# Kernel optimization log

Measured on AMD Instinct MI355X. Metric: run time of the kernel, lower is better.

The kernel has to match this reference:

```python
import jax, jax.numpy as jnp
import numpy as np

B, L, D, M = 4, 8192, 512, 256
EPS = 1e-6


def _feature_map(x, proj, is_query):
    # FAVOR+ positive softmax-kernel features.
    # x: (B, L, D), proj: (M, D) with orthogonal rows scaled by sqrt(D).
    d = x.shape[-1]
    xs = x * (d ** -0.25)                      # scale by d^{-1/4}
    dash = jnp.einsum('bld,md->blm', xs, proj)  # (B, L, M)
    diag = 0.5 * jnp.sum(xs * xs, axis=-1, keepdims=True)  # (B, L, 1)
    if is_query:
        stab = jnp.max(dash, axis=-1, keepdims=True)        # per-position max
    else:
        stab = jnp.max(dash, axis=(-2, -1), keepdims=True)  # per-batch max
    return jnp.exp(dash - diag - stab) / jnp.sqrt(jnp.asarray(M, x.dtype)) + EPS


def setup_inputs() -> dict:
    key = jax.random.key(0)
    kq, kk, kv, kp = jax.random.split(key, 4)
    Q = jax.random.normal(kq, (B, L, D), dtype=jnp.float32)
    K = jax.random.normal(kk, (B, L, D), dtype=jnp.float32)
    V = jax.random.normal(kv, (B, L, D), dtype=jnp.float32)
    # Orthogonal random projection: QR of a Gaussian, rows scaled by sqrt(D).
    G = jax.random.normal(kp, (D, M), dtype=jnp.float32)
    q, _ = jnp.linalg.qr(G)                     # (D, M), orthonormal columns
    proj = q.T * jnp.sqrt(jnp.asarray(D, jnp.float32))  # (M, D)
    return {"Q": Q, "K": K, "V": V, "proj": proj}


def reference(Q, K, V, proj):
    Qf = _feature_map(Q, proj, is_query=True)   # (B, L, M)
    Kf = _feature_map(K, proj, is_query=False)  # (B, L, M)
    # Linear attention: aggregate keys/values once, O(L*M*D).
    KV = jnp.einsum('blm,bld->bmd', Kf, V)      # (B, M, D)
    Ksum = jnp.sum(Kf, axis=1)                  # (B, M)
    Z = 1.0 / (jnp.einsum('blm,bm->bl', Qf, Ksum) + EPS)  # (B, L)
    out = jnp.einsum('blm,bmd->bld', Qf, KV) * Z[..., None]
    return out
```

## Files before the change

kernel.cpp:

```cpp
#include <hip/hip_runtime.h>
#include <math.h>

typedef unsigned short u16;
typedef unsigned int u32;
typedef __attribute__((ext_vector_type(8))) short bf16x8;
typedef __attribute__((ext_vector_type(4))) float f32x4;

#define SCALE_ 0.21022410381342864f
#define EPS_ 1e-6f
#define RSQM_ 0.0625f
#define L_ 8192
#define PL_OFF_ 131072
#define KVL_OFF_ 524288

__device__ __forceinline__ float bf2f(u16 h) {
    return __uint_as_float(((u32)h) << 16);
}
__device__ __forceinline__ u32 cvtpk(float x0, float x1) {
    u32 w;
    asm("v_cvt_pk_bf16_f32 %0, %1, %2" : "=v"(w) : "v"(x0), "v"(x1));
    return w;
}
__device__ __forceinline__ void split_pk(float x0, float x1, u32& hw, u32& lw) {
    hw = cvtpk(x0, x1);
    float h0 = __uint_as_float(hw << 16);
    float h1 = __uint_as_float(hw & 0xffff0000u);
    lw = cvtpk(x0 - h0, x1 - h1);
}
__device__ __forceinline__ u32 okey(float x) {
    u32 b = __float_as_uint(x);
    return (b & 0x80000000u) ? ~b : (b | 0x80000000u);
}
__device__ __forceinline__ float odec(u32 k) {
    return (k & 0x80000000u) ? __uint_as_float(k & 0x7fffffffu) : __uint_as_float(~k);
}

#define GLDS16(gsrc, ldst) \
    __builtin_amdgcn_global_load_lds((__attribute__((address_space(1))) void*)(gsrc), \
                                     (__attribute__((address_space(3))) void*)(ldst), 16, 0, 0)

__global__ __launch_bounds__(256) void split_p(const float* __restrict__ P,
        u16* __restrict__ Ph, u16* __restrict__ Pl, u32* __restrict__ bmax) {
    if (blockIdx.x == 0 && threadIdx.x < 4) bmax[threadIdx.x] = 0u;
    int i = (blockIdx.x * 256 + threadIdx.x) * 2;
    u32 hw, lw;
    split_pk(P[i] * SCALE_, P[i + 1] * SCALE_, hw, lw);
    *reinterpret_cast<u32*>(&Ph[i]) = hw;
    *reinterpret_cast<u32*>(&Pl[i]) = lw;
}

__global__ __launch_bounds__(256) void dash_all(
        const float* __restrict__ Qg, const float* __restrict__ Kg,
        const u16* __restrict__ Bh_g,
        u16* __restrict__ QF, u16* __restrict__ KfT, float* __restrict__ ksump,
        u32* __restrict__ bmax) {
    __shared__ __align__(16) u16 Ah[2][64 * 32], Al[2][64 * 32];
    __shared__ __align__(16) u16 Bh[2][256 * 32], Bl[2][256 * 32];
    const int qpath = !(blockIdx.x & 1);
    const int tile = blockIdx.x >> 1;
    const float* __restrict__ X = qpath ? Qg : Kg;
    const int t = threadIdx.x, lane = t & 63;
    const int wid = t >> 6;
    const int row0 = tile * 64;
    const int l15 = lane & 15, l4 = lane >> 4;
    const int sr = t >> 2;
    const int awz = sr * 32 + (((t & 3) ^ ((sr >> 1) & 3)) * 8);
    const int koff = (l4 ^ ((l15 >> 1) & 3)) * 8;
    float ss = 0.f;

    const float* xp = &X[(size_t)(row0 + sr) * 512 + (t & 3) * 8];
    const u16* bsrch[4];
#pragma unroll
    for (int it = 0; it < 4; ++it) {
        const int m = it * 64 + wid * 16 + (lane >> 2);
        const int swz = ((lane & 3) ^ ((m >> 1) & 3)) * 8;
        bsrch[it] = Bh_g + (size_t)m * 512 + swz;
    }

    f32x4 acc[4][4];
#pragma unroll
    for (int i = 0; i < 4; ++i)
#pragma unroll
        for (int j = 0; j < 4; ++j) acc[i][j] = (f32x4){0.f, 0.f, 0.f, 0.f};

    float4 v0 = *reinterpret_cast<const float4*>(xp);
    float4 v1 = *reinterpret_cast<const float4*>(xp + 4);
    float4 v2 = *reinterpret_cast<const float4*>(xp + 32);
    float4 v3 = *reinterpret_cast<const float4*>(xp + 36);

    for (int kt = 0; kt < 8; ++kt) {
        __syncthreads();
        {
#pragma unroll
            for (int it = 0; it < 4; ++it) {
                GLDS16(bsrch[it],                 &Bh[0][it * 2048 + wid * 512]);
                GLDS16(bsrch[it] + PL_OFF_,       &Bl[0][it * 2048 + wid * 512]);
                GLDS16(bsrch[it] + 32,            &Bh[1][it * 2048 + wid * 512]);
                GLDS16(bsrch[it] + 32 + PL_OFF_,  &Bl[1][it * 2048 + wid * 512]);
                bsrch[it] += 64;
            }
            float xs[8] = {v0.x, v0.y, v0.z, v0.w, v1.x, v1.y, v1.z, v1.w};
            float ys[8] = {v2.x, v2.y, v2.z, v2.w, v3.x, v3.y, v3.z, v3.w};
#pragma unroll
            for (int i = 0; i < 8; ++i) {
                ss = fmaf(xs[i], xs[i], ss);
                ss = fmaf(ys[i], ys[i], ss);
            }
            u32 hw[4], lw[4];
#pragma unroll
            for (int i = 0; i < 4; ++i) split_pk(xs[2 * i], xs[2 * i + 1], hw[i], lw[i]);
            *reinterpret_cast<uint4*>(&Ah[0][awz]) = make_uint4(hw[0], hw[1], hw[2], hw[3]);
            *reinterpret_cast<uint4*>(&Al[0][awz]) = make_uint4(lw[0], lw[1], lw[2], lw[3]);
#pragma unroll
            for (int i = 0; i < 4; ++i) split_pk(ys[2 * i], ys[2 * i + 1], hw[i], lw[i]);
            *reinterpret_cast<uint4*>(&Ah[1][awz]) = make_uint4(hw[0], hw[1], hw[2], hw[3]);
            *reinterpret_cast<uint4*>(&Al[1][awz]) = make_uint4(lw[0], lw[1], lw[2], lw[3]);
            xp = (kt < 7) ? xp + 64 : xp;
            v0 = *reinterpret_cast<const float4*>(xp);
            v1 = *reinterpret_cast<const float4*>(xp + 4);
            v2 = *reinterpret_cast<const float4*>(xp + 32);
            v3 = *reinterpret_cast<const float4*>(xp + 36);
        }
        __syncthreads();
#pragma unroll
        for (int h = 0; h < 2; ++h) {
            bf16x8 a_h[4], a_l[4];
#pragma unroll
            for (int mf = 0; mf < 4; ++mf) {
                int r = (mf * 16 + l15) * 32 + koff;
                a_h[mf] = *reinterpret_cast<const bf16x8*>(&Ah[h][r]);
                a_l[mf] = *reinterpret_cast<const bf16x8*>(&Al[h][r]);
            }
#pragma unroll
            for (int nf = 0; nf < 4; ++nf) {
                const int r = (wid * 64 + nf * 16 + l15) * 32 + koff;
                bf16x8 b_h = *reinterpret_cast<const bf16x8*>(&Bh[h][r]);
                bf16x8 b_l = *reinterpret_cast<const bf16x8*>(&Bl[h][r]);
#pragma unroll
                for (int mf = 0; mf < 4; ++mf) {
                    acc[mf][nf] = __builtin_amdgcn_mfma_f32_16x16x32_bf16(a_h[mf], b_h, acc[mf][nf], 0, 0, 0);
                    acc[mf][nf] = __builtin_amdgcn_mfma_f32_16x16x32_bf16(a_h[mf], b_l, acc[mf][nf], 0, 0, 0);
                    acc[mf][nf] = __builtin_amdgcn_mfma_f32_16x16x32_bf16(a_l[mf], b_h, acc[mf][nf], 0, 0, 0);
                }
            }
        }
    }
    __syncthreads();
    float* rmaxp = reinterpret_cast<float*>(&Ah[0][0]);
    float* diagp = reinterpret_cast<float*>(&Al[0][0]);

    ss += __shfl_xor(ss, 1);
    ss += __shfl_xor(ss, 2);
    if ((t & 3) == 0) diagp[sr] = 0.5f * SCALE_ * SCALE_ * ss;

    if (qpath) {
        float rm[4][4];
#pragma unroll
        for (int mf = 0; mf < 4; ++mf)
#pragma unroll
            for (int r = 0; r < 4; ++r) {
                float v = fmaxf(fmaxf(acc[mf][0][r], acc[mf][1][r]),
                                fmaxf(acc[mf][2][r], acc[mf][3][r]));
#pragma unroll
                for (int off = 1; off < 16; off <<= 1) v = fmaxf(v, __shfl_xor(v, off));
                rm[mf][r] = v;
            }
        if (l15 == 0) {
#pragma unroll
            for (int mf = 0; mf < 4; ++mf)
#pragma unroll
                for (int r = 0; r < 4; ++r)
                    rmaxp[(mf * 16 + l4 * 4 + r) * 4 + wid] = rm[mf][r];
        }
        __syncthreads();
#pragma unroll
        for (int mf = 0; mf < 4; ++mf)
#pragma unroll
            for (int r = 0; r < 4; ++r) {
                const int rl = mf * 16 + l4 * 4 + r;
                float m4 = fmaxf(fmaxf(rmaxp[rl * 4 + 0], rmaxp[rl * 4 + 1]),
                                 fmaxf(rmaxp[rl * 4 + 2], rmaxp[rl * 4 + 3]));
                const float c = diagp[rl] + m4;
                float f0 = expf(acc[mf][0][r] - c) * RSQM_ + EPS_;
                float f1 = expf(acc[mf][1][r] - c) * RSQM_ + EPS_;
                float f2 = expf(acc[mf][2][r] - c) * RSQM_ + EPS_;
                float f3 = expf(acc[mf][3][r] - c) * RSQM_ + EPS_;
                u32 w01 = cvtpk(f0, f1), w23 = cvtpk(f2, f3);
                size_t o = (size_t)(row0 + rl) * 256 + wid * 64 + l15;
                QF[o]      = (u16)w01;
                QF[o + 16] = (u16)(w01 >> 16);
                QF[o + 32] = (u16)w23;
                QF[o + 48] = (u16)(w23 >> 16);
            }
    } else {
        __syncthreads();
        const int b = row0 >> 13;
        const int ll = row0 & 8191;
        float bm = -1e30f;
        float s[4] = {0.f, 0.f, 0.f, 0.f};
#pragma unroll
        for (int nf = 0; nf < 4; ++nf) {
            const size_t mb = ((size_t)(b * 256 + wid * 64 + nf * 16 + l15)) * 8192 + ll + l4 * 4;
#pragma unroll
            for (int mf = 0; mf < 4; ++mf) {
                float e0 = acc[mf][nf][0], e1 = acc[mf][nf][1];
                float e2 = acc[mf][nf][2], e3 = acc[mf][nf][3];
                bm = fmaxf(fmaxf(bm, fmaxf(e0, e1)), fmaxf(e2, e3));
                float x0 = expf(e0 - diagp[mf * 16 + l4 * 4 + 0]);
                float x1 = expf(e1 - diagp[mf * 16 + l4 * 4 + 1]);
                float x2 = expf(e2 - diagp[mf * 16 + l4 * 4 + 2]);
                float x3 = expf(e3 - diagp[mf * 16 + l4 * 4 + 3]);
                s[nf] += (x0 + x1) + (x2 + x3);
                uint2 w = make_uint2(cvtpk(x0, x1), cvtpk(x2, x3));
                *reinterpret_cast<uint2*>(&KfT[mb + mf * 16]) = w;
            }
        }
#pragma unroll
        for (int nf = 0; nf < 4; ++nf) {
            s[nf] += __shfl_xor(s[nf], 16);
            s[nf] += __shfl_xor(s[nf], 32);
        }
        if (l4 == 0) {
#pragma unroll
            for (int nf = 0; nf < 4; ++nf)
                ksump[tile * 256 + wid * 64 + nf * 16 + l15] = s[nf];
        }
#pragma unroll
        for (int off = 1; off < 64; off <<= 1) bm = fmaxf(bm, __shfl_xor(bm, off));
        if (lane == 0) diagp[64 + wid] = bm;
        __syncthreads();
        if (t == 0) {
            float m = fmaxf(fmaxf(diagp[64], diagp[65]), fmaxf(diagp[66], diagp[67]));
            atomicMax(&bmax[b], okey(m));
        }
    }
}

__global__ __launch_bounds__(256) void split_vt(const float* __restrict__ V,
        u16* __restrict__ Vt, float* __restrict__ vsump) {
    const int dt = blockIdx.x & 7, lt = blockIdx.x >> 3;
    const int lg = lt * 64, b = lg >> 13, d0 = dt * 64;
    __shared__ u16 T[64][72];
    const int t = threadIdx.x;
    const int lrow = t >> 2, c0 = (t & 3) * 16;
#pragma unroll
    for (int ii = 0; ii < 4; ++ii) {
        float4 v = *reinterpret_cast<const float4*>(&V[(size_t)(lg + lrow) * 512 + d0 + c0 + ii * 4]);
        *reinterpret_cast<u32*>(&T[lrow][c0 + ii * 4 + 0]) = cvtpk(v.x, v.y);
        *reinterpret_cast<u32*>(&T[lrow][c0 + ii * 4 + 2]) = cvtpk(v.z, v.w);
    }
    __syncthreads();
    const int dloc = t >> 2, lc = (t & 3) * 16;
    u32 w[8];
    float s = 0.f;
#pragma unroll
    for (int j = 0; j < 8; ++j) {
        u16 a = T[lc + 2 * j][dloc], c = T[lc + 2 * j + 1][dloc];
        w[j] = (u32)a | ((u32)c << 16);
        s += bf2f(a) + bf2f(c);
    }
    size_t ob = ((size_t)(b * 512 + d0 + dloc)) * 8192 + (lg & 8191) + lc;
    reinterpret_cast<uint4*>(&Vt[ob])[0] = make_uint4(w[0], w[1], w[2], w[3]);
    reinterpret_cast<uint4*>(&Vt[ob])[1] = make_uint4(w[4], w[5], w[6], w[7]);
    s += __shfl_xor(s, 1);
    s += __shfl_xor(s, 2);
    if ((t & 3) == 0) vsump[lt * 512 + d0 + dloc] = s;
}

__global__ __launch_bounds__(256) void ksum_red(const float* __restrict__ ksump,
        const u32* __restrict__ bmax, float* __restrict__ KsumT) {
    const int wid = threadIdx.x >> 6, lane = threadIdx.x & 63;
    const int o = blockIdx.x * 4 + wid;
    const int b = o >> 8, m = o & 255;
    float s = ksump[(size_t)(b * 128 + lane) * 256 + m]
            + ksump[(size_t)(b * 128 + 64 + lane) * 256 + m];
#pragma unroll
    for (int off = 1; off < 64; off <<= 1) s += __shfl_xor(s, off);
    if (lane == 0) {
        const float g = expf(-odec(bmax[b]));
        KsumT[o] = g * s + (float)L_ * EPS_;
    }
}

__global__ __launch_bounds__(256) void vsum_red(const float* __restrict__ vsump,
        float* __restrict__ Vsum) {
    const int wid = threadIdx.x >> 6, lane = threadIdx.x & 63;
    const int o = blockIdx.x * 4 + wid;
    const int b = o >> 9, d = o & 511;
    float s = vsump[(size_t)(b * 128 + lane) * 512 + d]
            + vsump[(size_t)(b * 128 + 64 + lane) * 512 + d];
#pragma unroll
    for (int off = 1; off < 64; off <<= 1) s += __shfl_xor(s, off);
    if (lane == 0) Vsum[o] = s;
}

__global__ __launch_bounds__(256) void kv_mfma(
        const u16* __restrict__ KfT, const u16* __restrict__ Vt,
        float* __restrict__ kvp) {
    int o = (blockIdx.x & 7) * 64 + (blockIdx.x >> 3);
    const int dt = o & 3, mt = (o >> 2) & 1, ch = (o >> 3) & 15, b = o >> 7;
    const u16* Ag = KfT + ((size_t)(b * 256 + mt * 128)) * 8192 + ch * 512;
    const u16* Bg = Vt + ((size_t)(b * 512 + dt * 128)) * 8192 + ch * 512;
    __shared__ __align__(16) u16 A_[2][128 * 32], B_[2][128 * 32];
    const int t = threadIdx.x, lane = t & 63;
    const int wid = t >> 6, wr = wid >> 1, wc = wid & 1;
    const int l15 = lane & 15, l4 = lane >> 4;
    const int koff = (l4 ^ ((l15 >> 1) & 3)) * 8;
    const u16* asrc[2];
    const u16* bsrc[2];
#pragma unroll
    for (int it = 0; it < 2; ++it) {
        const int row = it * 64 + wid * 16 + (lane >> 2);
        const int swz = ((lane & 3) ^ ((row >> 1) & 3)) * 8;
        asrc[it] = Ag + (size_t)row * 8192 + swz;
        bsrc[it] = Bg + (size_t)row * 8192 + swz;
    }
    f32x4 acc[4][4];
#pragma unroll
    for (int i = 0; i < 4; ++i)
#pragma unroll
        for (int j = 0; j < 4; ++j) acc[i][j] = (f32x4){0.f, 0.f, 0.f, 0.f};

    for (int kt = 0; kt < 8; ++kt) {
        __syncthreads();
#pragma unroll
        for (int it = 0; it < 2; ++it) {
            GLDS16(asrc[it],      &A_[0][it * 2048 + wid * 512]);
            GLDS16(asrc[it] + 32, &A_[1][it * 2048 + wid * 512]);
            GLDS16(bsrc[it],      &B_[0][it * 2048 + wid * 512]);
            GLDS16(bsrc[it] + 32, &B_[1][it * 2048 + wid * 512]);
            asrc[it] += 64; bsrc[it] += 64;
        }
        __syncthreads();
#pragma unroll
        for (int h = 0; h < 2; ++h) {
            bf16x8 a[4];
#pragma unroll
            for (int mf = 0; mf < 4; ++mf)
                a[mf] = *reinterpret_cast<const bf16x8*>(&A_[h][(wr * 64 + mf * 16 + l15) * 32 + koff]);
#pragma unroll
            for (int nf = 0; nf < 4; ++nf) {
                bf16x8 bb = *reinterpret_cast<const bf16x8*>(&B_[h][(wc * 64 + nf * 16 + l15) * 32 + koff]);
#pragma unroll
                for (int mf = 0; mf < 4; ++mf)
                    acc[mf][nf] = __builtin_amdgcn_mfma_f32_16x16x32_bf16(a[mf], bb, acc[mf][nf], 0, 0, 0);
            }
        }
    }
#pragma unroll
    for (int mf = 0; mf < 4; ++mf)
#pragma unroll
        for (int r = 0; r < 4; ++r) {
            size_t oo = ((size_t)(ch * 4 + b) * 256 + mt * 128 + wr * 64 + mf * 16 + l4 * 4 + r) * 512
                        + dt * 128 + wc * 64;
#pragma unroll
            for (int nf = 0; nf < 4; ++nf)
                kvp[oo + nf * 16 + l15] = acc[mf][nf][r];
        }
}

__global__ __launch_bounds__(256) void kv_fix(const float* __restrict__ kvp,
        const u32* __restrict__ bmax, const float* __restrict__ Vsum,
        u16* __restrict__ KVth, u16* __restrict__ KVtl) {
    const int dt = blockIdx.x & 7, mt = (blockIdx.x >> 3) & 3, b = blockIdx.x >> 5;
    const int m0 = mt * 64, d0 = dt * 64;
    __shared__ u16 Th[64][72], Tl[64][72];
    const int t = threadIdx.x, mloc = t >> 2, c0 = (t & 3) * 16;
    float s[16];
#pragma unroll
    for (int j = 0; j < 16; ++j) s[j] = 0.f;
    for (int c = 0; c < 16; ++c) {
        size_t base = ((size_t)(c * 4 + b) * 256 + m0 + mloc) * 512 + d0 + c0;
#pragma unroll
        for (int ii = 0; ii < 4; ++ii) {
            float4 v = *reinterpret_cast<const float4*>(&kvp[base + ii * 4]);
            s[ii * 4 + 0] += v.x; s[ii * 4 + 1] += v.y;
            s[ii * 4 + 2] += v.z; s[ii * 4 + 3] += v.w;
        }
    }
    const float g = expf(-odec(bmax[b]));
#pragma unroll
    for (int j = 0; j < 16; j += 2) {
        float v0 = g * s[j]     + EPS_ * Vsum[b * 512 + d0 + c0 + j];
        float v1 = g * s[j + 1] + EPS_ * Vsum[b * 512 + d0 + c0 + j + 1];
        u32 hw, lw; split_pk(v0, v1, hw, lw);
        *reinterpret_cast<u32*>(&Th[mloc][c0 + j]) = hw;
        *reinterpret_cast<u32*>(&Tl[mloc][c0 + j]) = lw;
    }
    __syncthreads();
    const int dloc = t >> 2, mc = (t & 3) * 16;
    size_t ob = ((size_t)(b * 512 + d0 + dloc)) * 256 + m0 + mc;
    u32 wh[8], wl[8];
#pragma unroll
    for (int j = 0; j < 8; ++j) {
        wh[j] = (u32)Th[mc + 2 * j][dloc] | ((u32)Th[mc + 2 * j + 1][dloc] << 16);
        wl[j] = (u32)Tl[mc + 2 * j][dloc] | ((u32)Tl[mc + 2 * j + 1][dloc] << 16);
    }
    reinterpret_cast<uint4*>(&KVth[ob])[0] = make_uint4(wh[0], wh[1], wh[2], wh[3]);
    reinterpret_cast<uint4*>(&KVth[ob])[1] = make_uint4(wh[4], wh[5], wh[6], wh[7]);
    reinterpret_cast<uint4*>(&KVtl[ob])[0] = make_uint4(wl[0], wl[1], wl[2], wl[3]);
    reinterpret_cast<uint4*>(&KVtl[ob])[1] = make_uint4(wl[4], wl[5], wl[6], wl[7]);
}

__global__ __launch_bounds__(256) void z_kernel(const u16* __restrict__ QF,
        const float* __restrict__ KsumT, float* __restrict__ Z) {
    const int wid = threadIdx.x >> 6, lane = threadIdx.x & 63;
    const int row = blockIdx.x * 4 + wid;
    const int b = row >> 13;
    uint2 u = *reinterpret_cast<const uint2*>(&QF[(size_t)row * 256 + lane * 4]);
    float4 ks = *reinterpret_cast<const float4*>(&KsumT[b * 256 + lane * 4]);
    float s = bf2f((u16)(u.x & 0xffff)) * ks.x + bf2f((u16)(u.x >> 16)) * ks.y +
              bf2f((u16)(u.y & 0xffff)) * ks.z + bf2f((u16)(u.y >> 16)) * ks.w;
#pragma unroll
    for (int off = 1; off < 64; off <<= 1) s += __shfl_xor(s, off);
    if (lane == 0) Z[row] = 1.f / (s + EPS_);
}

__global__ __launch_bounds__(256) void out_mfma(
        const u16* __restrict__ QF, const u16* __restrict__ KVth,
        const float* __restrict__ Z, float* __restrict__ out) {
    int o = (blockIdx.x & 7) * 128 + (blockIdx.x >> 3);
    const int dt = o & 3, rt = o >> 2;
    const int row0 = rt * 128, b = row0 >> 13;
    const u16* Ag = QF + (size_t)row0 * 256;
    const u16* Bh_g = KVth + ((size_t)(b * 512 + dt * 128)) * 256;
    __shared__ __align__(16) u16 A_[2][128 * 32], Bh_[2][128 * 32], Bl_[2][128 * 32];
    const int t = threadIdx.x, lane = t & 63;
    const int wid = t >> 6, wr = wid >> 1, wc = wid & 1;
    const int l15 = lane & 15, l4 = lane >> 4;
    const int koff = (l4 ^ ((l15 >> 1) & 3)) * 8;
    const u16* asrc[2];
    const u16* bhsrc[2];
#pragma unroll
    for (int it = 0; it < 2; ++it) {
        const int row = it * 64 + wid * 16 + (lane >> 2);
        const int swz = ((lane & 3) ^ ((row >> 1) & 3)) * 8;
        asrc[it]  = Ag + (size_t)row * 256 + swz;
        bhsrc[it] = Bh_g + (size_t)row * 256 + swz;
    }
    f32x4 acc[4][4];
#pragma unroll
    for (int i = 0; i < 4; ++i)
#pragma unroll
        for (int j = 0; j < 4; ++j) acc[i][j] = (f32x4){0.f, 0.f, 0.f, 0.f};

    for (int kt = 0; kt < 4; ++kt) {
        __syncthreads();
#pragma unroll
        for (int it = 0; it < 2; ++it) {
            GLDS16(asrc[it],                  &A_[0][it * 2048 + wid * 512]);
            GLDS16(asrc[it] + 32,             &A_[1][it * 2048 + wid * 512]);
            GLDS16(bhsrc[it],                 &Bh_[0][it * 2048 + wid * 512]);
            GLDS16(bhsrc[it] + 32,            &Bh_[1][it * 2048 + wid * 512]);
            GLDS16(bhsrc[it] + KVL_OFF_,      &Bl_[0][it * 2048 + wid * 512]);
            GLDS16(bhsrc[it] + 32 + KVL_OFF_, &Bl_[1][it * 2048 + wid * 512]);
            asrc[it] += 64; bhsrc[it] += 64;
        }
        __syncthreads();
#pragma unroll
        for (int h = 0; h < 2; ++h) {
            bf16x8 a[4];
#pragma unroll
            for (int mf = 0; mf < 4; ++mf)
                a[mf] = *reinterpret_cast<const bf16x8*>(&A_[h][(wr * 64 + mf * 16 + l15) * 32 + koff]);
#pragma unroll
            for (int nf = 0; nf < 4; ++nf) {
                const int r = (wc * 64 + nf * 16 + l15) * 32 + koff;
                bf16x8 bh = *reinterpret_cast<const bf16x8*>(&Bh_[h][r]);
                bf16x8 bl = *reinterpret_cast<const bf16x8*>(&Bl_[h][r]);
#pragma unroll
                for (int mf = 0; mf < 4; ++mf) {
                    acc[mf][nf] = __builtin_amdgcn_mfma_f32_16x16x32_bf16(a[mf], bh, acc[mf][nf], 0, 0, 0);
                    acc[mf][nf] = __builtin_amdgcn_mfma_f32_16x16x32_bf16(a[mf], bl, acc[mf][nf], 0, 0, 0);
                }
            }
        }
    }
#pragma unroll
    for (int mf = 0; mf < 4; ++mf)
#pragma unroll
        for (int r = 0; r < 4; ++r) {
            const int row = row0 + wr * 64 + mf * 16 + l4 * 4 + r;
            const float z = Z[row];
#pragma unroll
            for (int nf = 0; nf < 4; ++nf)
                out[(size_t)row * 512 + dt * 128 + wc * 64 + nf * 16 + l15] = acc[mf][nf][r] * z;
        }
}

extern "C" void kernel_launch(void* const* d_in, const int* in_sizes, int n_in,
                              void* d_out, int out_size, void* d_ws, size_t ws_size,
                              hipStream_t stream) {
    const float* Q = (const float*)d_in[0];
    const float* K = (const float*)d_in[1];
    const float* V = (const float*)d_in[2];
    const float* P = (const float*)d_in[3];
    float* out = (float*)d_out;
    char* ws = (char*)d_ws;

    u16*   QF    = (u16*)(ws + 0);
    u16*   KfT   = (u16*)(ws + 16777216);
    u16*   Vt    = (u16*)(ws + 33554432);
    float* kvp   = (float*)(ws + 67108864);
    u16*   KVth  = (u16*)(ws + 100663296);
    u16*   KVtl  = (u16*)(ws + 101711872);
    u16*   PH    = (u16*)(ws + 102760448);
    u16*   PL    = (u16*)(ws + 103022592);
    float* ksump = (float*)(ws + 103284736);
    float* vsump = (float*)(ws + 103809024);
    float* KsumT = (float*)(ws + 104857600);
    float* Vsum  = (float*)(ws + 104861696);
    float* Zbuf  = (float*)(ws + 104869888);
    u32*   bmax  = (u32*)(ws + 105000960);

    split_p<<<256, 256, 0, stream>>>(P, PH, PL, bmax);
    dash_all<<<1024, 256, 0, stream>>>(Q, K, PH, QF, KfT, ksump, bmax);
    split_vt<<<4096, 256, 0, stream>>>(V, Vt, vsump);
    ksum_red<<<256, 256, 0, stream>>>(ksump, bmax, KsumT);
    vsum_red<<<512, 256, 0, stream>>>(vsump, Vsum);
    kv_mfma<<<512, 256, 0, stream>>>(KfT, Vt, kvp);
    kv_fix<<<128, 256, 0, stream>>>(kvp, bmax, Vsum, KVth, KVtl);
    z_kernel<<<8192, 256, 0, stream>>>(QF, KsumT, Zbuf);
    out_mfma<<<1024, 256, 0, stream>>>(QF, KVth, Zbuf, out);
}
```

Baseline: 160.8 us.

## Fuse V transpose/bf16 conversion and V-sum into kv_mfma B-tile loading

Removes the separate split_vt kernel that transposed V into a bf16 Vt buffer. kv_mfma now reads fp32 V directly, converts pairs to bf16 and writes them swizzled into the LDS B tile, while also accumulating per-column V sums. A small vsum_red reduces the per-chunk partials. This eliminates a full write and re-read of the transposed V (about 32 MB of traffic) and one launch. In exchange, the B-tile load becomes synchronous register loads with scattered 4-byte LDS stores instead of async global-to-LDS copies, and V is read twice, once by each mt tile.

```diff
diff --git a/kernel.cpp b/kernel.cpp
--- a/kernel.cpp
+++ b/kernel.cpp
@@ -236,37 +236,6 @@
     }
 }
 
-__global__ __launch_bounds__(256) void split_vt(const float* __restrict__ V,
-        u16* __restrict__ Vt, float* __restrict__ vsump) {
-    const int dt = blockIdx.x & 7, lt = blockIdx.x >> 3;
-    const int lg = lt * 64, b = lg >> 13, d0 = dt * 64;
-    __shared__ u16 T[64][72];
-    const int t = threadIdx.x;
-    const int lrow = t >> 2, c0 = (t & 3) * 16;
-#pragma unroll
-    for (int ii = 0; ii < 4; ++ii) {
-        float4 v = *reinterpret_cast<const float4*>(&V[(size_t)(lg + lrow) * 512 + d0 + c0 + ii * 4]);
-        *reinterpret_cast<u32*>(&T[lrow][c0 + ii * 4 + 0]) = cvtpk(v.x, v.y);
-        *reinterpret_cast<u32*>(&T[lrow][c0 + ii * 4 + 2]) = cvtpk(v.z, v.w);
-    }
-    __syncthreads();
-    const int dloc = t >> 2, lc = (t & 3) * 16;
-    u32 w[8];
-    float s = 0.f;
-#pragma unroll
-    for (int j = 0; j < 8; ++j) {
-        u16 a = T[lc + 2 * j][dloc], c = T[lc + 2 * j + 1][dloc];
-        w[j] = (u32)a | ((u32)c << 16);
-        s += bf2f(a) + bf2f(c);
-    }
-    size_t ob = ((size_t)(b * 512 + d0 + dloc)) * 8192 + (lg & 8191) + lc;
-    reinterpret_cast<uint4*>(&Vt[ob])[0] = make_uint4(w[0], w[1], w[2], w[3]);
-    reinterpret_cast<uint4*>(&Vt[ob])[1] = make_uint4(w[4], w[5], w[6], w[7]);
-    s += __shfl_xor(s, 1);
-    s += __shfl_xor(s, 2);
-    if ((t & 3) == 0) vsump[lt * 512 + d0 + dloc] = s;
-}
-
 __global__ __launch_bounds__(256) void ksum_red(const float* __restrict__ ksump,
         const u32* __restrict__ bmax, float* __restrict__ KsumT) {
     const int wid = threadIdx.x >> 6, lane = threadIdx.x & 63;
@@ -282,39 +251,29 @@
     }
 }
 
-__global__ __launch_bounds__(256) void vsum_red(const float* __restrict__ vsump,
-        float* __restrict__ Vsum) {
-    const int wid = threadIdx.x >> 6, lane = threadIdx.x & 63;
-    const int o = blockIdx.x * 4 + wid;
-    const int b = o >> 9, d = o & 511;
-    float s = vsump[(size_t)(b * 128 + lane) * 512 + d]
-            + vsump[(size_t)(b * 128 + 64 + lane) * 512 + d];
-#pragma unroll
-    for (int off = 1; off < 64; off <<= 1) s += __shfl_xor(s, off);
-    if (lane == 0) Vsum[o] = s;
-}
-
 __global__ __launch_bounds__(256) void kv_mfma(
-        const u16* __restrict__ KfT, const u16* __restrict__ Vt,
-        float* __restrict__ kvp) {
+        const u16* __restrict__ KfT, const float* __restrict__ V,
+        float* __restrict__ kvp, float* __restrict__ vsump) {
     int o = (blockIdx.x & 7) * 64 + (blockIdx.x >> 3);
     const int dt = o & 3, mt = (o >> 2) & 1, ch = (o >> 3) & 15, b = o >> 7;
     const u16* Ag = KfT + ((size_t)(b * 256 + mt * 128)) * 8192 + ch * 512;
-    const u16* Bg = Vt + ((size_t)(b * 512 + dt * 128)) * 8192 + ch * 512;
+    const float* Vg = V + ((size_t)(b * 8192 + ch * 512)) * 512 + dt * 128;
     __shared__ __align__(16) u16 A_[2][128 * 32], B_[2][128 * 32];
     const int t = threadIdx.x, lane = t & 63;
     const int wid = t >> 6, wr = wid >> 1, wc = wid & 1;
     const int l15 = lane & 15, l4 = lane >> 4;
     const int koff = (l4 ^ ((l15 >> 1) & 3)) * 8;
     const u16* asrc[2];
-    const u16* bsrc[2];
 #pragma unroll
     for (int it = 0; it < 2; ++it) {
         const int row = it * 64 + wid * 16 + (lane >> 2);
         const int swz = ((lane & 3) ^ ((row >> 1) & 3)) * 8;
         asrc[it] = Ag + (size_t)row * 8192 + swz;
-        bsrc[it] = Bg + (size_t)row * 8192 + swz;
-    }
+    }
+    const int dq = t >> 3;
+    const int lpb = (t & 7) * 2;
+    float vs[4] = {0.f, 0.f, 0.f, 0.f};
+
     f32x4 acc[4][4];
 #pragma unroll
     for (int i = 0; i < 4; ++i)
@@ -327,10 +286,29 @@
         for (int it = 0; it < 2; ++it) {
             GLDS16(asrc[it],      &A_[0][it * 2048 + wid * 512]);
             GLDS16(asrc[it] + 32, &A_[1][it * 2048 + wid * 512]);
-            GLDS16(bsrc[it],      &B_[0][it * 2048 + wid * 512]);
-            GLDS16(bsrc[it] + 32, &B_[1][it * 2048 + wid * 512]);
-            asrc[it] += 64; bsrc[it] += 64;
-        }
+            asrc[it] += 64;
+        }
+#pragma unroll
+        for (int h = 0; h < 2; ++h)
+#pragma unroll
+            for (int j = 0; j < 2; ++j) {
+                const int lp = lpb + j;
+                const int l = kt * 64 + h * 32 + lp * 2;
+                const float* vp = Vg + (size_t)l * 512 + dq * 4;
+                float4 va = *reinterpret_cast<const float4*>(vp);
+                float4 vb = *reinterpret_cast<const float4*>(vp + 512);
+                const int lo = lp * 2;
+                const int lblk = lo >> 3, lin = lo & 7;
+                float av[4] = {va.x, va.y, va.z, va.w};
+                float bv[4] = {vb.x, vb.y, vb.z, vb.w};
+#pragma unroll
+                for (int d = 0; d < 4; ++d) {
+                    const int drow = dq * 4 + d;
+                    const int ls = (lblk ^ ((drow >> 1) & 3)) * 8 + lin;
+                    *reinterpret_cast<u32*>(&B_[h][drow * 32 + ls]) = cvtpk(av[d], bv[d]);
+                    vs[d] += av[d] + bv[d];
+                }
+            }
         __syncthreads();
 #pragma unroll
         for (int h = 0; h < 2; ++h) {
@@ -346,6 +324,16 @@
                     acc[mf][nf] = __builtin_amdgcn_mfma_f32_16x16x32_bf16(a[mf], bb, acc[mf][nf], 0, 0, 0);
             }
         }
+    }
+#pragma unroll
+    for (int d = 0; d < 4; ++d) {
+        vs[d] += __shfl_xor(vs[d], 1);
+        vs[d] += __shfl_xor(vs[d], 2);
+        vs[d] += __shfl_xor(vs[d], 4);
+    }
+    if (mt == 0 && (t & 7) == 0) {
+        float4 w = make_float4(vs[0], vs[1], vs[2], vs[3]);
+        *reinterpret_cast<float4*>(&vsump[(size_t)ch * 2048 + b * 512 + dt * 128 + dq * 4]) = w;
     }
 #pragma unroll
     for (int mf = 0; mf < 4; ++mf)
@@ -357,6 +345,15 @@
             for (int nf = 0; nf < 4; ++nf)
                 kvp[oo + nf * 16 + l15] = acc[mf][nf][r];
         }
+}
+
+__global__ __launch_bounds__(256) void vsum_red(const float* __restrict__ vsump,
+        float* __restrict__ Vsum) {
+    const int o = blockIdx.x * 256 + threadIdx.x;
+    float s = 0.f;
+#pragma unroll
+    for (int c = 0; c < 16; ++c) s += vsump[(size_t)c * 2048 + o];
+    Vsum[o] = s;
 }
 
 __global__ __launch_bounds__(256) void kv_fix(const float* __restrict__ kvp,
@@ -500,25 +497,23 @@
 
     u16*   QF    = (u16*)(ws + 0);
     u16*   KfT   = (u16*)(ws + 16777216);
-    u16*   Vt    = (u16*)(ws + 33554432);
-    float* kvp   = (float*)(ws + 67108864);
-    u16*   KVth  = (u16*)(ws + 100663296);
-    u16*   KVtl  = (u16*)(ws + 101711872);
-    u16*   PH    = (u16*)(ws + 102760448);
-    u16*   PL    = (u16*)(ws + 103022592);
-    float* ksump = (float*)(ws + 103284736);
-    float* vsump = (float*)(ws + 103809024);
-    float* KsumT = (float*)(ws + 104857600);
-    float* Vsum  = (float*)(ws + 104861696);
-    float* Zbuf  = (float*)(ws + 104869888);
-    u32*   bmax  = (u32*)(ws + 105000960);
+    float* kvp   = (float*)(ws + 33554432);
+    u16*   KVth  = (u16*)(ws + 67108864);
+    u16*   KVtl  = (u16*)(ws + 68157440);
+    u16*   PH    = (u16*)(ws + 69206016);
+    u16*   PL    = (u16*)(ws + 69468160);
+    float* ksump = (float*)(ws + 69730304);
+    float* vsump = (float*)(ws + 70254592);
+    float* KsumT = (float*)(ws + 70385664);
+    float* Vsum  = (float*)(ws + 70389760);
+    float* Zbuf  = (float*)(ws + 70397952);
+    u32*   bmax  = (u32*)(ws + 70529024);
 
     split_p<<<256, 256, 0, stream>>>(P, PH, PL, bmax);
     dash_all<<<1024, 256, 0, stream>>>(Q, K, PH, QF, KfT, ksump, bmax);
-    split_vt<<<4096, 256, 0, stream>>>(V, Vt, vsump);
     ksum_red<<<256, 256, 0, stream>>>(ksump, bmax, KsumT);
-    vsum_red<<<512, 256, 0, stream>>>(vsump, Vsum);
-    kv_mfma<<<512, 256, 0, stream>>>(KfT, Vt, kvp);
+    kv_mfma<<<512, 256, 0, stream>>>(KfT, V, kvp, vsump);
+    vsum_red<<<8, 256, 0, stream>>>(vsump, Vsum);
     kv_fix<<<128, 256, 0, stream>>>(kvp, bmax, Vsum, KVth, KVtl);
     z_kernel<<<8192, 256, 0, stream>>>(QF, KsumT, Zbuf);
     out_mfma<<<1024, 256, 0, stream>>>(QF, KVth, Zbuf, out);
```

New measurement: 151.9 us (median of 2 runs). 5.6% less time.
